# Optimization experiments

Hardware: AMD Instinct MI355X
Metric: run time of the kernel (lower is better)

The kernel has to match this reference:

```python
import jax, jax.numpy as jnp
import numpy as np

DIM = 192
HEADS = 8
B, H, W = 8, 128, 128


def _split_heads(t, heads):
    # [b, n, c] -> [b, heads, c//heads, n]
    b, n, c = t.shape
    t = t.reshape(b, n, heads, c // heads)
    return jnp.transpose(t, (0, 2, 3, 1))


def _l2norm(t):
    # normalize along last (token) dim, matching F.normalize eps=1e-12
    n = jnp.linalg.norm(t, axis=-1, keepdims=True)
    return t / jnp.maximum(n, 1e-12)


def setup_inputs() -> dict:
    key = jax.random.key(0)
    ks = jax.random.split(key, 12)
    s = 1.0 / np.sqrt(DIM)
    inp = {
        "x1": jax.random.normal(ks[0], (B, DIM, H, W), jnp.float32),
        "x2": jax.random.normal(ks[1], (B, DIM, H, W), jnp.float32),
        "q1": jax.random.normal(ks[2], (B, DIM, H, W), jnp.float32),
        "q2": jax.random.normal(ks[3], (B, DIM, H, W), jnp.float32),
        "Wq": jax.random.normal(ks[4], (DIM, DIM), jnp.float32) * s,
        "bq": jax.random.normal(ks[5], (DIM,), jnp.float32) * s,
        "Wk": jax.random.normal(ks[6], (DIM, DIM), jnp.float32) * s,
        "bk": jax.random.normal(ks[7], (DIM,), jnp.float32) * s,
        "Wv": jax.random.normal(ks[8], (DIM, DIM), jnp.float32) * s,
        "bv": jax.random.normal(ks[9], (DIM,), jnp.float32) * s,
        "scale": jnp.ones((HEADS, 1, 1), jnp.float32),
        "Wproj": jax.random.normal(ks[10], (DIM, DIM), jnp.float32) * s,
    }
    return inp


def reference(x1, x2, q1, q2, Wq, bq, Wk, bk, Wv, bv, scale, Wproj):
    b, c, h, w = x1.shape
    heads = HEADS

    def flat(t):  # b c h w -> b (h w) c
        return jnp.transpose(t.reshape(b, c, h * w), (0, 2, 1))

    x1f, x2f, q1f, q2f = flat(x1), flat(x2), flat(q1), flat(q2)

    # NOTE: faithful to source: q2 uses q_proj1; k2/v2 use k_proj1/v_proj1
    q1p = q1f @ Wq.T + bq
    q2p = q2f @ Wq.T + bq
    k1 = x1f @ Wk.T + bk
    v1 = x1f @ Wv.T + bv
    k2 = x2f @ Wk.T + bk
    v2 = x2f @ Wv.T + bv

    q1h = _l2norm(_split_heads(q1p, heads))  # [b, head, hd, n]
    q2h = _l2norm(_split_heads(q2p, heads))
    k1h = _l2norm(_split_heads(k1, heads))
    k2h = _l2norm(_split_heads(k2, heads))
    v1h = _split_heads(v1, heads)
    v2h = _split_heads(v2, heads)

    # channel attention: [b, head, hd, hd]
    attn1 = jax.nn.softmax(jnp.einsum('bhcn,bhdn->bhcd', q1h, k2h) * scale, axis=-1)
    out1 = jnp.einsum('bhcd,bhdn->bhcn', attn1, v2h)
    attn2 = jax.nn.softmax(jnp.einsum('bhcn,bhdn->bhcd', q2h, k1h) * scale, axis=-1)
    out2 = jnp.einsum('bhcd,bhdn->bhcn', attn2, v1h)

    def merge(t):  # [b, head, hd, n] -> [b, c, h, w]
        return t.reshape(b, c, h, w)

    out1 = jnp.einsum('oc,bchw->bohw', Wproj, merge(out1))
    out2 = jnp.einsum('oc,bchw->bohw', Wproj, merge(out2))
    return (out1, out2)
```

## Files before the change

kernel.cpp:

```cpp
#include <hip/hip_runtime.h>
#include <hip/hip_bf16.h>
#include <math.h>

using bf16 = __hip_bfloat16;
typedef __attribute__((ext_vector_type(8))) short short8;
typedef __attribute__((ext_vector_type(4))) float f32x4;

static __device__ __forceinline__ float b2f(bf16 x) { return __bfloat162float(x); }
static __device__ __forceinline__ bf16 f2b(float x) { return __float2bfloat16(x); }
static __device__ __forceinline__ short f2bs(float x) {
  bf16 h = __float2bfloat16(x);
  return *reinterpret_cast<short*>(&h);
}
static __device__ __forceinline__ short8 load8_f2b(const float* p) {
  float4 a = *reinterpret_cast<const float4*>(p);
  float4 b = *reinterpret_cast<const float4*>(p + 4);
  short8 r;
  r[0] = f2bs(a.x); r[1] = f2bs(a.y); r[2] = f2bs(a.z); r[3] = f2bs(a.w);
  r[4] = f2bs(b.x); r[5] = f2bs(b.y); r[6] = f2bs(b.z); r[7] = f2bs(b.w);
  return r;
}

#define MFMA16(a, b, c) __builtin_amdgcn_mfma_f32_16x16x32_bf16((a), (b), (c), 0, 0, 0)

#define NB 8
#define CDIM 192
#define NTOK 16384
#define CN ((size_t)CDIM * NTOK)

struct GemmParams {
  const float *q1, *q2, *x1, *x2;
  const float *Wq, *Wk, *bq, *bk;
  bf16* proj;
  const bf16* M;
  const float* Bf;
  float* out;
  int mode;
};

__global__ __launch_bounds__(256, 2) void gemm_oc(GemmParams P) {
  const int tid = threadIdx.x;
  const int z = blockIdx.y;

  const float* Xf;
  const float* Wf = nullptr;
  const bf16* Wb = nullptr;
  const float* bias;
  bf16* OUTb = nullptr;
  float* OUTf = nullptr;

  if (P.mode == 0) {
    int b = z >> 2, p = z & 3;
    Xf = (p == 0 ? P.q1 : p == 1 ? P.q2 : p == 2 ? P.x1 : P.x2) + (size_t)b * CN;
    Wf = (p < 2) ? P.Wq : P.Wk;
    bias = (p < 2) ? P.bq : P.bk;
    OUTb = P.proj + (size_t)(p * 8 + b) * CN;
  } else {
    Wb = P.M + (size_t)z * (CDIM * CDIM);
    bias = P.Bf + z * CDIM;
    Xf = (((z >> 3) == 0) ? P.x2 : P.x1) + (size_t)(z & 7) * CN;
    OUTf = P.out + (size_t)z * CN;
  }

  const int n0 = blockIdx.x * 64;

  __shared__ __align__(16) bf16 Bs[64 * 200];
  for (int ch = tid; ch < 3072; ch += 256) {
    int c = ch >> 4, jc = ch & 15;
    float4 v = *reinterpret_cast<const float4*>(Xf + (size_t)c * NTOK + n0 + jc * 4);
    Bs[(jc * 4 + 0) * 200 + c] = f2b(v.x);
    Bs[(jc * 4 + 1) * 200 + c] = f2b(v.y);
    Bs[(jc * 4 + 2) * 200 + c] = f2b(v.z);
    Bs[(jc * 4 + 3) * 200 + c] = f2b(v.w);
  }
  __syncthreads();

  const int wave = tid >> 6, lane = tid & 63;
  const int quad = lane >> 4, l15 = lane & 15;
  const int mb = wave * 48;

  f32x4 acc[3][4];
#pragma unroll
  for (int i = 0; i < 3; i++)
#pragma unroll
    for (int j = 0; j < 4; j++) acc[i][j] = (f32x4){0.f, 0.f, 0.f, 0.f};

#pragma unroll
  for (int ks = 0; ks < 6; ks++) {
    const int k0 = ks * 32 + quad * 8;
    short8 a[3], bb[4];
#pragma unroll
    for (int mt = 0; mt < 3; mt++) {
      const int row = mb + mt * 16 + l15;
      if (P.mode == 0) a[mt] = load8_f2b(Wf + (size_t)row * CDIM + k0);
      else             a[mt] = *reinterpret_cast<const short8*>(Wb + (size_t)row * CDIM + k0);
    }
#pragma unroll
    for (int nt = 0; nt < 4; nt++)
      bb[nt] = *reinterpret_cast<const short8*>(&Bs[(nt * 16 + l15) * 200 + k0]);
#pragma unroll
    for (int mt = 0; mt < 3; mt++)
#pragma unroll
      for (int nt = 0; nt < 4; nt++) acc[mt][nt] = MFMA16(a[mt], bb[nt], acc[mt][nt]);
  }

#pragma unroll
  for (int mt = 0; mt < 3; mt++) {
    const int obase = mb + mt * 16 + quad * 4;
    float bias4[4];
#pragma unroll
    for (int r = 0; r < 4; r++) bias4[r] = bias[obase + r];
#pragma unroll
    for (int nt = 0; nt < 4; nt++)
#pragma unroll
      for (int r = 0; r < 4; r++) {
        const size_t idx = (size_t)(obase + r) * NTOK + n0 + nt * 16 + l15;
        const float val = acc[mt][nt][r] + bias4[r];
        if (P.mode == 0) OUTb[idx] = f2b(val);
        else             OUTf[idx] = val;
      }
  }
}

__global__ __launch_bounds__(256, 2) void gram48(const bf16* __restrict__ proj,
                                                 float* __restrict__ Gbuf) {
  const int blk = blockIdx.x;
  const int ks = blk & 3, h = (blk >> 2) & 7, b = (blk >> 5) & 7, p = blk >> 8;

  const bf16* qsel = proj + (size_t)((p == 0 ? 0 : 1) * 8 + b) * CN + (size_t)h * 24 * NTOK;
  const bf16* ksel = proj + (size_t)((p == 0 ? 3 : 2) * 8 + b) * CN + (size_t)h * 24 * NTOK;

  const int tid = threadIdx.x, wave = tid >> 6, lane = tid & 63;
  const int quad = lane >> 4, l15 = lane & 15;

  const bf16* rp[3];
#pragma unroll
  for (int mt = 0; mt < 3; mt++) {
    int r = mt * 16 + l15;
    rp[mt] = (r < 24) ? qsel + (size_t)r * NTOK : ksel + (size_t)(r - 24) * NTOK;
  }

  f32x4 acc[3][3];
#pragma unroll
  for (int i = 0; i < 3; i++)
#pragma unroll
    for (int j = 0; j < 3; j++) acc[i][j] = (f32x4){0.f, 0.f, 0.f, 0.f};

  const int kend = ks * 4096 + 4096;
#pragma unroll 2
  for (int k = ks * 4096 + wave * 32 + quad * 8; k < kend; k += 128) {
    short8 f[3];
#pragma unroll
    for (int mt = 0; mt < 3; mt++) f[mt] = *reinterpret_cast<const short8*>(rp[mt] + k);
#pragma unroll
    for (int i = 0; i < 3; i++)
#pragma unroll
      for (int j = 0; j < 3; j++) acc[i][j] = MFMA16(f[i], f[j], acc[i][j]);
  }

  __shared__ float Gs[48 * 48];
  for (int i = tid; i < 2304; i += 256) Gs[i] = 0.f;
  __syncthreads();
#pragma unroll
  for (int i = 0; i < 3; i++)
#pragma unroll
    for (int j = 0; j < 3; j++)
#pragma unroll
      for (int r = 0; r < 4; r++)
        atomicAdd(&Gs[(i * 16 + quad * 4 + r) * 48 + j * 16 + l15], acc[i][j][r]);
  __syncthreads();

  float* gout = Gbuf + (size_t)((p * 8 + b) * 8 + h) * 2304;
  for (int i = tid; i < 2304; i += 256) atomicAdd(gout + i, Gs[i]);
}

__global__ void attn_softmax(const float* __restrict__ Gbuf, const float* __restrict__ scale,
                             float* __restrict__ Abuf) {
  const int blk = blockIdx.x;
  const int h = blk & 7;
  const float* G = Gbuf + (size_t)blk * 2304;
  __shared__ float nrm[48];
  const int t = threadIdx.x;
  if (t < 48) nrm[t] = sqrtf(fmaxf(G[t * 48 + t], 0.f));
  __syncthreads();
  if (t < 24) {
    const float scl = scale[h];
    const float nq = fmaxf(nrm[t], 1e-12f);
    float lg[24], mx = -1e30f;
#pragma unroll
    for (int d = 0; d < 24; d++) {
      lg[d] = G[t * 48 + 24 + d] / (nq * fmaxf(nrm[24 + d], 1e-12f)) * scl;
      mx = fmaxf(mx, lg[d]);
    }
    float s = 0.f;
#pragma unroll
    for (int d = 0; d < 24; d++) { lg[d] = expf(lg[d] - mx); s += lg[d]; }
    const float inv = 1.f / s;
    float* Ao = Abuf + (size_t)blk * 576 + t * 24;
#pragma unroll
    for (int d = 0; d < 24; d++) Ao[d] = lg[d] * inv;
  }
}

__global__ __launch_bounds__(256) void fold_M(const float* __restrict__ Abuf,
                                              const float* __restrict__ Wproj,
                                              const float* __restrict__ Wv,
                                              const float* __restrict__ bv,
                                              bf16* __restrict__ Mbuf,
                                              float* __restrict__ Bbuf) {
  const int blk = blockIdx.x;
  const int pb = blk / 12, ot = blk % 12;
  const int tid = threadIdx.x;

  __shared__ float As[4608];
  __shared__ float Wps[3072];
  __shared__ float Ts[3072];
  __shared__ float bvs[192];

  for (int i = tid; i < 4608; i += 256) As[i] = Abuf[(size_t)pb * 4608 + i];
  for (int i = tid; i < 3072; i += 256)
    Wps[i] = Wproj[(size_t)(ot * 16 + i / 192) * CDIM + (i % 192)];
  if (tid < 192) bvs[tid] = bv[tid];
  __syncthreads();

  for (int idx = tid; idx < 3072; idx += 256) {
    const int tr = idx / 192, cp = idx % 192;
    const int h = cp / 24, d = cp % 24;
    const float* Ah = &As[h * 576 + d];
    const float* Wr = &Wps[tr * 192 + h * 24];
    float s = 0.f;
#pragma unroll
    for (int cl = 0; cl < 24; cl++) s += Wr[cl] * Ah[cl * 24];
    Ts[idx] = s;
  }
  __syncthreads();

  for (int idx = tid; idx < 3072; idx += 256) {
    const int tr = idx / 192, e = idx % 192;
    const float* Tr = &Ts[tr * 192];
    float s = 0.f;
#pragma unroll 8
    for (int cp = 0; cp < 192; cp++) s += Tr[cp] * Wv[(size_t)cp * CDIM + e];
    Mbuf[((size_t)pb * CDIM + ot * 16 + tr) * CDIM + e] = f2b(s);
  }
  if (tid < 16) {
    const float* Tr = &Ts[tid * 192];
    float s = 0.f;
#pragma unroll 8
    for (int cp = 0; cp < 192; cp++) s += Tr[cp] * bvs[cp];
    Bbuf[pb * CDIM + ot * 16 + tid] = s;
  }
}

extern "C" void kernel_launch(void* const* d_in, const int* in_sizes, int n_in,
                              void* d_out, int out_size, void* d_ws, size_t ws_size,
                              hipStream_t stream) {
  const float* x1 = (const float*)d_in[0];
  const float* x2 = (const float*)d_in[1];
  const float* q1 = (const float*)d_in[2];
  const float* q2 = (const float*)d_in[3];
  const float* Wq = (const float*)d_in[4];
  const float* bq = (const float*)d_in[5];
  const float* Wk = (const float*)d_in[6];
  const float* bk = (const float*)d_in[7];
  const float* Wv = (const float*)d_in[8];
  const float* bv = (const float*)d_in[9];
  const float* scale = (const float*)d_in[10];
  const float* Wproj = (const float*)d_in[11];

  char* ws = (char*)d_ws;
  const size_t proj_bytes = (size_t)4 * 8 * CN * 2;
  const size_t gbuf_bytes = (size_t)2 * 8 * 8 * 2304 * 4;
  const size_t abuf_bytes = (size_t)2 * 8 * 8 * 576 * 4;
  const size_t mbuf_bytes = (size_t)16 * 192 * 192 * 2;

  bf16* proj = (bf16*)ws;
  float* Gbuf = (float*)(ws + proj_bytes);
  float* Abuf = (float*)(ws + proj_bytes + gbuf_bytes);
  bf16* Mbuf = (bf16*)(ws + proj_bytes + gbuf_bytes + abuf_bytes);
  float* Bbuf = (float*)(ws + proj_bytes + gbuf_bytes + abuf_bytes + mbuf_bytes);

  hipMemsetAsync(Gbuf, 0, gbuf_bytes, stream);

  GemmParams P;
  P.q1 = q1; P.q2 = q2; P.x1 = x1; P.x2 = x2;
  P.Wq = Wq; P.Wk = Wk; P.bq = bq; P.bk = bk;
  P.proj = proj; P.M = Mbuf; P.Bf = Bbuf; P.out = (float*)d_out;
  P.mode = 0;

  gemm_oc<<<dim3(256, 32), 256, 0, stream>>>(P);
  gram48<<<dim3(512), 256, 0, stream>>>(proj, Gbuf);
  attn_softmax<<<dim3(128), 64, 0, stream>>>(Gbuf, scale, Abuf);
  fold_M<<<dim3(192), 256, 0, stream>>>(Abuf, Wproj, Wv, bv, Mbuf, Bbuf);
  GemmParams P2 = P; P2.mode = 1;
  gemm_oc<<<dim3(256, 16), 256, 0, stream>>>(P2);
}
```

Measured before the change: 840.3 us.

## Pre-convert QK weights to bf16, swap MFMA operands for vectorized stores

Adds a small kernel that converts Wq and Wk to bf16 once, storing them in the Abuf workspace before attention reuses that space. This removes the per-block fp32-to-bf16 weight conversion inside the projection GEMM. The GEMM now puts tokens in the A operand and weights in the B operand, so each lane holds four consecutive tokens and can write 4-wide vector stores instead of scalar ones. The input tile load is also restructured into wider transposing stores into shared memory, and launch bounds are raised to 4 blocks per CU, which tightens the register budget.

After: 771.9 us. -8.1%, faster.

```diff
diff --git a/kernel.cpp b/kernel.cpp
--- a/kernel.cpp
+++ b/kernel.cpp
@@ -4,22 +4,14 @@
 
 using bf16 = __hip_bfloat16;
 typedef __attribute__((ext_vector_type(8))) short short8;
+typedef __attribute__((ext_vector_type(4))) short short4v;
 typedef __attribute__((ext_vector_type(4))) float f32x4;
 
-static __device__ __forceinline__ float b2f(bf16 x) { return __bfloat162float(x); }
 static __device__ __forceinline__ bf16 f2b(float x) { return __float2bfloat16(x); }
 static __device__ __forceinline__ short f2bs(float x) {
   bf16 h = __float2bfloat16(x);
   return *reinterpret_cast<short*>(&h);
 }
-static __device__ __forceinline__ short8 load8_f2b(const float* p) {
-  float4 a = *reinterpret_cast<const float4*>(p);
-  float4 b = *reinterpret_cast<const float4*>(p + 4);
-  short8 r;
-  r[0] = f2bs(a.x); r[1] = f2bs(a.y); r[2] = f2bs(a.z); r[3] = f2bs(a.w);
-  r[4] = f2bs(b.x); r[5] = f2bs(b.y); r[6] = f2bs(b.z); r[7] = f2bs(b.w);
-  return r;
-}
 
 #define MFMA16(a, b, c) __builtin_amdgcn_mfma_f32_16x16x32_bf16((a), (b), (c), 0, 0, 0)
 
@@ -28,9 +20,21 @@
 #define NTOK 16384
 #define CN ((size_t)CDIM * NTOK)
 
+__global__ __launch_bounds__(256) void convert_w(const float* __restrict__ Wq,
+                                                 const float* __restrict__ Wk,
+                                                 bf16* __restrict__ Wqk) {
+  const int e = (blockIdx.x * 256 + threadIdx.x) * 4;
+  const float* src = (e < CDIM * CDIM) ? (Wq + e) : (Wk + (e - CDIM * CDIM));
+  f32x4 v = *reinterpret_cast<const f32x4*>(src);
+  short4v w;
+  w[0] = f2bs(v[0]); w[1] = f2bs(v[1]); w[2] = f2bs(v[2]); w[3] = f2bs(v[3]);
+  *reinterpret_cast<short4v*>(Wqk + e) = w;
+}
+
 struct GemmParams {
   const float *q1, *q2, *x1, *x2;
-  const float *Wq, *Wk, *bq, *bk;
+  const bf16* Wqk;
+  const float *bq, *bk;
   bf16* proj;
   const bf16* M;
   const float* Bf;
@@ -38,21 +42,20 @@
   int mode;
 };
 
-__global__ __launch_bounds__(256, 2) void gemm_oc(GemmParams P) {
+__global__ __launch_bounds__(256, 4) void gemm_oc(GemmParams P) {
   const int tid = threadIdx.x;
   const int z = blockIdx.y;
 
   const float* Xf;
-  const float* Wf = nullptr;
-  const bf16* Wb = nullptr;
+  const bf16* Wb;
   const float* bias;
   bf16* OUTb = nullptr;
   float* OUTf = nullptr;
 
   if (P.mode == 0) {
-    int b = z >> 2, p = z & 3;
+    const int b = z >> 2, p = z & 3;
     Xf = (p == 0 ? P.q1 : p == 1 ? P.q2 : p == 2 ? P.x1 : P.x2) + (size_t)b * CN;
-    Wf = (p < 2) ? P.Wq : P.Wk;
+    Wb = P.Wqk + ((p < 2) ? 0 : CDIM * CDIM);
     bias = (p < 2) ? P.bq : P.bk;
     OUTb = P.proj + (size_t)(p * 8 + b) * CN;
   } else {
@@ -64,61 +67,85 @@
 
   const int n0 = blockIdx.x * 64;
 
-  __shared__ __align__(16) bf16 Bs[64 * 200];
-  for (int ch = tid; ch < 3072; ch += 256) {
-    int c = ch >> 4, jc = ch & 15;
-    float4 v = *reinterpret_cast<const float4*>(Xf + (size_t)c * NTOK + n0 + jc * 4);
-    Bs[(jc * 4 + 0) * 200 + c] = f2b(v.x);
-    Bs[(jc * 4 + 1) * 200 + c] = f2b(v.y);
-    Bs[(jc * 4 + 2) * 200 + c] = f2b(v.z);
-    Bs[(jc * 4 + 3) * 200 + c] = f2b(v.w);
-  }
-  __syncthreads();
-
-  const int wave = tid >> 6, lane = tid & 63;
+  __shared__ __align__(16) bf16 Xs[64 * 200];
+
+  {
+    const int c0 = (tid & 15) * 4;
+    const int t0 = (tid >> 4) * 4;
+    f32x4 v[3][4];
+#pragma unroll
+    for (int cb = 0; cb < 3; cb++)
+#pragma unroll
+      for (int i = 0; i < 4; i++)
+        v[cb][i] = *reinterpret_cast<const f32x4*>(
+            Xf + (size_t)(cb * 64 + c0 + i) * NTOK + n0 + t0);
+#pragma unroll
+    for (int cb = 0; cb < 3; cb++) {
+#pragma unroll
+      for (int j = 0; j < 4; j++) {
+        short4v w;
+        w[0] = f2bs(v[cb][0][j]);
+        w[1] = f2bs(v[cb][1][j]);
+        w[2] = f2bs(v[cb][2][j]);
+        w[3] = f2bs(v[cb][3][j]);
+        *reinterpret_cast<short4v*>(&Xs[(t0 + j) * 200 + cb * 64 + c0]) = w;
+      }
+    }
+  }
+  __syncthreads();
+
+  const int lane = tid & 63, wave = tid >> 6;
   const int quad = lane >> 4, l15 = lane & 15;
-  const int mb = wave * 48;
-
-  f32x4 acc[3][4];
-#pragma unroll
-  for (int i = 0; i < 3; i++)
-#pragma unroll
-    for (int j = 0; j < 4; j++) acc[i][j] = (f32x4){0.f, 0.f, 0.f, 0.f};
+  const int ob = wave * 48;
+
+  f32x4 acc[4][3];
+#pragma unroll
+  for (int t = 0; t < 4; t++)
+#pragma unroll
+    for (int ot = 0; ot < 3; ot++) acc[t][ot] = (f32x4){0.f, 0.f, 0.f, 0.f};
+
+  const bf16* W0 = Wb + (size_t)(ob + l15) * CDIM;
 
 #pragma unroll
   for (int ks = 0; ks < 6; ks++) {
     const int k0 = ks * 32 + quad * 8;
-    short8 a[3], bb[4];
-#pragma unroll
-    for (int mt = 0; mt < 3; mt++) {
-      const int row = mb + mt * 16 + l15;
-      if (P.mode == 0) a[mt] = load8_f2b(Wf + (size_t)row * CDIM + k0);
-      else             a[mt] = *reinterpret_cast<const short8*>(Wb + (size_t)row * CDIM + k0);
+    short8 xf[4], wf[3];
+#pragma unroll
+    for (int t = 0; t < 4; t++)
+      xf[t] = *reinterpret_cast<const short8*>(&Xs[(t * 16 + l15) * 200 + k0]);
+#pragma unroll
+    for (int ot = 0; ot < 3; ot++)
+      wf[ot] = *reinterpret_cast<const short8*>(W0 + (size_t)ot * 16 * CDIM + k0);
+#pragma unroll
+    for (int t = 0; t < 4; t++)
+#pragma unroll
+      for (int ot = 0; ot < 3; ot++) acc[t][ot] = MFMA16(xf[t], wf[ot], acc[t][ot]);
+  }
+
+#pragma unroll
+  for (int ot = 0; ot < 3; ot++) {
+    const int o = ob + ot * 16 + l15;
+    const float bo = bias[o];
+    if (P.mode == 0) {
+      bf16* dst = OUTb + (size_t)o * NTOK + n0 + quad * 4;
+#pragma unroll
+      for (int t = 0; t < 4; t++) {
+        short4v w;
+        w[0] = f2bs(acc[t][ot][0] + bo);
+        w[1] = f2bs(acc[t][ot][1] + bo);
+        w[2] = f2bs(acc[t][ot][2] + bo);
+        w[3] = f2bs(acc[t][ot][3] + bo);
+        *reinterpret_cast<short4v*>(dst + t * 16) = w;
+      }
+    } else {
+      float* dst = OUTf + (size_t)o * NTOK + n0 + quad * 4;
+#pragma unroll
+      for (int t = 0; t < 4; t++) {
+        f32x4 w = {acc[t][ot][0] + bo, acc[t][ot][1] + bo,
+                   acc[t][ot][2] + bo, acc[t][ot][3] + bo};
+        *reinterpret_cast<f32x4*>(dst + t * 16) = w;
+      }
     }
-#pragma unroll
-    for (int nt = 0; nt < 4; nt++)
-      bb[nt] = *reinterpret_cast<const short8*>(&Bs[(nt * 16 + l15) * 200 + k0]);
-#pragma unroll
-    for (int mt = 0; mt < 3; mt++)
-#pragma unroll
-      for (int nt = 0; nt < 4; nt++) acc[mt][nt] = MFMA16(a[mt], bb[nt], acc[mt][nt]);
-  }
-
-#pragma unroll
-  for (int mt = 0; mt < 3; mt++) {
-    const int obase = mb + mt * 16 + quad * 4;
-    float bias4[4];
-#pragma unroll
-    for (int r = 0; r < 4; r++) bias4[r] = bias[obase + r];
-#pragma unroll
-    for (int nt = 0; nt < 4; nt++)
-#pragma unroll
-      for (int r = 0; r < 4; r++) {
-        const size_t idx = (size_t)(obase + r) * NTOK + n0 + nt * 16 + l15;
-        const float val = acc[mt][nt][r] + bias4[r];
-        if (P.mode == 0) OUTb[idx] = f2b(val);
-        else             OUTf[idx] = val;
-      }
   }
 }
 
@@ -279,12 +306,16 @@
   float* Abuf = (float*)(ws + proj_bytes + gbuf_bytes);
   bf16* Mbuf = (bf16*)(ws + proj_bytes + gbuf_bytes + abuf_bytes);
   float* Bbuf = (float*)(ws + proj_bytes + gbuf_bytes + abuf_bytes + mbuf_bytes);
+  bf16* Wqk = (bf16*)(ws + proj_bytes + gbuf_bytes);
+  Wqk = (bf16*)Abuf;
 
   hipMemsetAsync(Gbuf, 0, gbuf_bytes, stream);
+
+  convert_w<<<dim3(72), 256, 0, stream>>>(Wq, Wk, Wqk);
 
   GemmParams P;
   P.q1 = q1; P.q2 = q2; P.x1 = x1; P.x2 = x2;
-  P.Wq = Wq; P.Wk = Wk; P.bq = bq; P.bk = bk;
+  P.Wqk = Wqk; P.bq = bq; P.bk = bk;
   P.proj = proj; P.M = Mbuf; P.Bf = Bbuf; P.out = (float*)d_out;
   P.mode = 0;
 
```
